# Optimization experiments

Measured on AMD Instinct MI355X. Metric: run time of the kernel, lower is better.

Reference implementation:

```python
import jax, jax.numpy as jnp
import numpy as np

_HMT = np.array([[1, 1, 1, 1], [1, -1, 1, -1], [1, 1, -1, -1], [1, -1, -1, 1]], dtype=np.float32)
_H = jnp.asarray(_HMT)
_H2 = jnp.asarray(_HMT[[1, 0, 2, 3], :])
_H3 = jnp.asarray(_HMT[[3, 1, 2, 0], :])
# inverse-transform rows 1:3 (2x4), reconstructed from truncated source
_IH = _H[1:3, :]
_IH2 = _H2[1:3, :]
_IH3 = _H3[1:3, :]

KERNEL = 4
STRIDE = 2


def setup_inputs() -> dict:
    key = jax.random.key(0)
    k1, k2, k3 = jax.random.split(key, 3)
    B, Cin, Cout, ih, iw = 16, 64, 96, 128, 128
    x = jax.random.normal(k1, (B, Cin, ih, iw), dtype=jnp.float32)
    weight = jax.random.normal(k2, (Cout, Cin, KERNEL, KERNEL), dtype=jnp.float32) * 0.05
    bias = jax.random.normal(k3, (1, Cout, 1, 1), dtype=jnp.float32) * 0.05
    return {"x": x, "weight": weight, "bias": bias}


def _extract_patches(xp, nH, nW):
    # patches[b,c,i,j,u,v] = xp[b,c, 2i+v, 2j+u]  (torch unfold(3).unfold(2) order)
    idx_h = 2 * np.arange(nH)[:, None] + np.arange(KERNEL)[None, :]  # (nH,4) over (i,v)
    idx_w = 2 * np.arange(nW)[:, None] + np.arange(KERNEL)[None, :]  # (nW,4) over (j,u)
    return xp[:, :, idx_h[:, None, None, :], idx_w[None, :, :, None]]  # (B,C,nH,nW,4,4)


def _group(t, w, ih_mat):
    # t: (B,C,nH,nW,4,4) transform-domain patches; w: (Og,C,4,4)
    m = jnp.einsum('bcijuv,ocuv->boijuv', t, w)
    # IH @ m @ IH.T -> (B,Og,nH,nW,2,2)
    return jnp.einsum('pu,boijuv,qv->boijpq', ih_mat, m, ih_mat)


def reference(x, weight, bias):
    B, Cin, ih, iw = x.shape
    Cout = weight.shape[0]
    nH, nW = ih // STRIDE, iw // STRIDE
    xp = jnp.pad(x, ((0, 0), (0, 0), (1, 1), (1, 1)))
    patches = _extract_patches(xp, nH, nW)
    # forward transforms: H @ P @ H ; H2.T @ P @ H2 ; H3.T @ P @ H3
    t1 = jnp.einsum('au,bcijuv,vd->bcijad', _H, patches, _H)
    t2 = jnp.einsum('ua,bcijuv,vd->bcijad', _H2, patches, _H2)
    t3 = jnp.einsum('ua,bcijuv,vd->bcijad', _H3, patches, _H3)
    g = Cout // 3
    h1 = _group(t1, weight[:g], _IH)
    h2 = _group(t2, weight[g:2 * g], _IH2)
    h3 = _group(t3, weight[2 * g:], _IH3)
    hmult = jnp.concatenate([h1, h2, h3], axis=1)  # (B,Cout,nH,nW,2,2)
    # out[b,o,2i+p,2j+q] = hmult[b,o,i,j,p,q]
    out = hmult.transpose(0, 1, 2, 4, 3, 5).reshape(B, Cout, ih, iw)
    return out + bias
```

## Files before the change

kernel.cpp:

```cpp
#include <hip/hip_runtime.h>
#include <hip/hip_bf16.h>
#include <cstddef>
#include <cstdint>


#define IHW 128
#define CIN 64
#define COUT 96
#define NCK 16

typedef __attribute__((ext_vector_type(8))) short short8_t;
typedef __attribute__((ext_vector_type(4))) float floatx4;

__device__ __forceinline__ short bf16r(float f) {
  uint32_t u = __float_as_uint(f);
  uint32_t r = (u + 0x7FFFu + ((u >> 16) & 1u)) >> 16;
  return (short)r;
}

__device__ __forceinline__ uint32_t pk(float lo, float hi) {
  union { __hip_bfloat16 h; unsigned short s; } a, bq;
  a.h = __float2bfloat16(lo);
  bq.h = __float2bfloat16(hi);
  return (uint32_t)a.s | ((uint32_t)bq.s << 16);
}

__global__ void keff_kernel(const float* __restrict__ w, short* __restrict__ keff) {
  int idx = blockIdx.x * 256 + threadIdx.x;
  if (idx >= COUT * CIN) return;
  int o = idx / CIN, c = idx % CIN;
  int g = o / 32;

  int perm[4] = {0, 1, 2, 3};
  if (g == 1) { perm[0] = 1; perm[1] = 0; }
  else if (g == 2) { perm[0] = 3; perm[3] = 0; }

  const float H[4][4] = {{1,1,1,1},{1,-1,1,-1},{1,1,-1,-1},{1,-1,-1,1}};
  float S[2][4];
#pragma unroll
  for (int p = 0; p < 2; ++p)
#pragma unroll
    for (int a = 0; a < 4; ++a) {
      bool pos = (g == 1) ? ((p == 0) ? true : (a < 2))
                          : ((p == 0) ? ((a & 1) == 0) : (a < 2));
      S[p][a] = pos ? 1.f : -1.f;
    }

  float wv[4][4];
#pragma unroll
  for (int a = 0; a < 4; ++a)
#pragma unroll
    for (int d = 0; d < 4; ++d) wv[a][d] = w[(o * CIN + c) * 16 + a * 4 + d];

  for (int p = 0; p < 2; ++p)
    for (int q = 0; q < 2; ++q) {
      int n = o * 4 + p * 2 + q;
      for (int y = 0; y < 4; ++y)
        for (int xx = 0; xx < 4; ++xx) {
          float s = 0.f;
#pragma unroll
          for (int a = 0; a < 4; ++a) {
            float ea = S[p][a] * H[a][perm[xx]];
#pragma unroll
            for (int d = 0; d < 4; ++d) s += ea * S[q][d] * H[d][perm[y]] * wv[a][d];
          }
          keff[n * 1024 + c * 16 + y * 4 + xx] = bf16r(s);
        }
    }
}

__global__ __launch_bounds__(256) void prepass(const float* __restrict__ x,
                                               uint32_t* __restrict__ img) {
  const int t = blockIdx.x * 256 + threadIdx.x;
  const int r = t >> 5;
  const int l = t & 31;
  const int py = r % 130;
  const int rc = r / 130;

  uint32_t d0 = 0, d1 = 0, t0 = 0;
  if (py != 0 && py != 129) {
    const float4 v = *reinterpret_cast<const float4*>(
        x + ((size_t)rc * IHW + (py - 1)) * IHW + 4 * l);
    float prev = __shfl_up(v.w, 1, 32);
    if (l == 0) prev = 0.f;
    d0 = pk(prev, v.x);
    d1 = pk(v.y, v.z);
    t0 = pk(v.w, 0.f);
  }
  uint32_t* row = img + (size_t)r * 68;
  *reinterpret_cast<uint2*>(row + 2 * l) = make_uint2(d0, d1);
  if (l == 31) *reinterpret_cast<uint4*>(row + 64) = make_uint4(t0, 0, 0, 0);
}

#define XBUF_DW 1632
#define ABUF_DW 4096

__global__ __launch_bounds__(256) void conv_mfma(const uint32_t* __restrict__ img,
                                                 const short* __restrict__ keff,
                                                 const float* __restrict__ bias,
                                                 float* __restrict__ out) {
  __shared__ uint32_t xlds[2 * XBUF_DW];
  __shared__ uint32_t alds[2 * ABUF_DW];

  const int tid = threadIdx.x;
  const int lane = tid & 63;
  const int wid = tid >> 6;
  const int wavem = wid >> 1;
  const int wn = wid & 1;
  const int l15 = lane & 15;
  const int l4 = lane >> 4;

  const int hw = blockIdx.x;
  const int xcd = hw & 7;
  const int r = hw >> 3;
  const int tile = xcd * 64 + r / 3;
  const int nblk = r % 3;
  const int b = tile >> 5;
  const int ib = tile & 31;

  const uint32_t* imgb = img + (size_t)b * CIN * 130 * 68;

  int xsrc[2];
  bool xok[2];
#pragma unroll
  for (int it = 0; it < 2; ++it) {
    const int u = wid * 102 + lane + it * 64;
    const int ri = u / 17;
    const int col16 = u % 17;
    const int kk = ri / 12;
    const int rem = ri % 12;
    const int y = rem >> 1;
    const int cs = rem & 1;
    const int cl = 2 * kk + cs;
    xsrc[it] = (cl * 130 + 4 * ib + y) * 68 + col16 * 4;
    xok[it] = (it == 0) || (lane < 38);
  }

  int aoff[4];
#pragma unroll
  for (int it = 0; it < 4; ++it) {
    const int slot = tid + it * 256;
    const int n = slot >> 3;
    const int u = slot & 7;
    aoff[it] = (nblk * 128 + n) * 1024 + ((u ^ (n & 7)) << 3);
  }

#define STAGE(bs, ckv)                                                     \
  {                                                                        \
    _Pragma("unroll") for (int it = 0; it < 4; ++it) {                     \
      const short* src = keff + aoff[it] + (ckv) * 64;                     \
      __builtin_amdgcn_global_load_lds(                                    \
          (const __attribute__((address_space(1))) void*)src,              \
          (__attribute__((address_space(3))) void*)                        \
              &alds[(bs) * ABUF_DW + (tid + it * 256) * 4],                \
          16, 0, 0);                                                       \
    }                                                                      \
    _Pragma("unroll") for (int it = 0; it < 2; ++it) {                     \
      if (xok[it]) {                                                       \
        const uint32_t* src = imgb + xsrc[it] + (ckv) * (4 * 130 * 68);    \
        __builtin_amdgcn_global_load_lds(                                  \
            (const __attribute__((address_space(1))) void*)src,            \
            (__attribute__((address_space(3))) void*)                      \
                &xlds[(bs) * XBUF_DW + (wid * 102 + it * 64) * 4],         \
            16, 0, 0);                                                     \
      }                                                                    \
    }                                                                      \
  }

  union ufrag { short8_t s8; uint32_t u[4]; };

  floatx4 acc[4][4];
#pragma unroll
  for (int i2 = 0; i2 < 4; ++i2)
#pragma unroll
    for (int j2 = 0; j2 < 4; ++j2) acc[i2][j2] = (floatx4){0.f, 0.f, 0.f, 0.f};

  float biasr[4];
#pragma unroll
  for (int nf = 0; nf < 4; ++nf) biasr[nf] = bias[nblk * 32 + wn * 16 + nf * 4 + l4];

  const int xbase = (4 * wavem + 4 * (l4 & 1) + (l4 >> 1)) * 68 + l15;
  const int abase = (wn * 64 + l15) * 32 + ((l4 ^ (l15 & 7)) << 2);

#define COMPUTE(ckv)                                                       \
  {                                                                        \
    const uint32_t* Ap = alds + ((ckv) & 1) * ABUF_DW;                     \
    const uint32_t* Xp = xlds + ((ckv) & 1) * XBUF_DW + xbase;             \
    _Pragma("unroll") for (int kk = 0; kk < 2; ++kk) {                     \
      short8_t af[4];                                                      \
      _Pragma("unroll") for (int nf = 0; nf < 4; ++nf)                     \
        af[nf] = *reinterpret_cast<const short8_t*>(                       \
            Ap + (abase ^ (kk << 4)) + nf * 512);                          \
      const uint32_t* Xk = Xp + kk * 816;                                  \
      ufrag xf[4];                                                         \
      _Pragma("unroll") for (int mf = 0; mf < 4; ++mf) {                   \
        const int o = mf * 16;                                             \
        xf[mf].u[0] = Xk[o];                                               \
        xf[mf].u[1] = Xk[o + 1];                                           \
        xf[mf].u[2] = Xk[o + 136];                                         \
        xf[mf].u[3] = Xk[o + 137];                                         \
      }                                                                    \
      _Pragma("unroll") for (int mf = 0; mf < 4; ++mf)                     \
        _Pragma("unroll") for (int nf = 0; nf < 4; ++nf)                   \
          acc[mf][nf] = __builtin_amdgcn_mfma_f32_16x16x32_bf16(           \
              af[nf], xf[mf].s8, acc[mf][nf], 0, 0, 0);                    \
    }                                                                      \
  }

  STAGE(0, 0);
  STAGE(1, 1);

  for (int ck = 0; ck < NCK - 1; ++ck) {
    asm volatile("s_waitcnt vmcnt(6) lgkmcnt(0)" ::: "memory");
    __builtin_amdgcn_s_barrier();
    __builtin_amdgcn_sched_barrier(0);
    COMPUTE(ck);
    if (ck + 2 < NCK) {
      __builtin_amdgcn_s_barrier();
      __builtin_amdgcn_sched_barrier(0);
      STAGE(ck & 1, ck + 2);
    }
  }
  asm volatile("s_waitcnt vmcnt(0) lgkmcnt(0)" ::: "memory");
  __builtin_amdgcn_s_barrier();
  __builtin_amdgcn_sched_barrier(0);
  COMPUTE(NCK - 1);

  const int i_row = ib * 2 + wavem;
  const int orow0 = 2 * i_row;
#pragma unroll
  for (int nf = 0; nf < 4; ++nf) {
    const int o = nblk * 32 + wn * 16 + nf * 4 + l4;
    const float bv = biasr[nf];
    float* obase = out + ((size_t)(b * COUT + o) * IHW + orow0) * IHW;
#pragma unroll
    for (int mf = 0; mf < 4; ++mf) {
      const int col = 2 * (mf * 16 + l15);
      float2 s0 = make_float2(acc[mf][nf][0] + bv, acc[mf][nf][1] + bv);
      float2 s1 = make_float2(acc[mf][nf][2] + bv, acc[mf][nf][3] + bv);
      *reinterpret_cast<float2*>(obase + col) = s0;
      *reinterpret_cast<float2*>(obase + IHW + col) = s1;
    }
  }
#undef STAGE
#undef COMPUTE
}

#define FB_P_DW 168
#define FB_COFF 80
#define FB_XBUF (12 * FB_P_DW)

__global__ __launch_bounds__(256) void conv_fb(const float* __restrict__ x,
                                               const short* __restrict__ keff,
                                               const float* __restrict__ bias,
                                               float* __restrict__ out) {
  __shared__ uint32_t xlds[2 * FB_XBUF];
  __shared__ uint32_t alds[2 * ABUF_DW];

  const int tid = threadIdx.x;
  const int lane = tid & 63;
  const int wid = tid >> 6;
  const int wavem = wid >> 1;
  const int wn = wid & 1;
  const int l15 = lane & 15;
  const int l4 = lane >> 4;

  const int hw = blockIdx.x;
  const int xcd = hw & 7;
  const int r = hw >> 3;
  const int tile = xcd * 64 + r / 3;
  const int nblk = r % 3;
  const int b = tile >> 5;
  const int ib = tile & 31;
  const int gy0 = ib * 4 - 1;

  const float* xb = x + (size_t)b * CIN * IHW * IHW;

  int sl_off[3], sl_dw[3], sl_s[3];
  bool sl_ok[3];
#pragma unroll
  for (int it = 0; it < 3; ++it) {
    const int slot = tid + it * 256;
    const int seg = slot >> 5;
    const int s = slot & 31;
    const int c_sub = seg / 12;
    const int rr = seg % 12;
    const int kk2 = rr / 6;
    const int y = rr % 6;
    const int c_loc = 2 * kk2 + c_sub;
    const int gy = gy0 + y;
    const bool ok = (unsigned)gy < (unsigned)IHW;
    sl_off[it] = (c_loc * IHW + (ok ? gy : 0)) * IHW + 4 * s;
    sl_dw[it] = rr * FB_P_DW + c_sub * FB_COFF;
    sl_s[it] = s;
    sl_ok[it] = ok;
  }

  int aoff[4];
#pragma unroll
  for (int it = 0; it < 4; ++it) {
    const int slot = tid + it * 256;
    const int n = slot >> 3;
    const int u = slot & 7;
    aoff[it] = (nblk * 128 + n) * 1024 + ((u ^ (n & 7)) << 3);
  }

  float4 gv[3];
  float gn[3];
#define FISSUE(ckv)                                                       \
  {                                                                       \
    _Pragma("unroll") for (int it = 0; it < 3; ++it) {                    \
      const float* p = xb + sl_off[it] + (size_t)(ckv) * (4 * IHW * IHW); \
      gv[it] = *reinterpret_cast<const float4*>(p);                       \
      gn[it] = (sl_s[it] < 31) ? p[4] : 0.f;                              \
    }                                                                     \
  }
#define FWRITE(bs)                                                        \
  {                                                                       \
    uint32_t* Bp = xlds + (bs) * FB_XBUF;                                 \
    _Pragma("unroll") for (int it = 0; it < 3; ++it) {                    \
      float4 v = gv[it];                                                  \
      float nx = gn[it];                                                  \
      if (!sl_ok[it]) { v.x = 0.f; v.y = 0.f; v.z = 0.f; v.w = 0.f; nx = 0.f; } \
      const int o = sl_dw[it] + 2 * sl_s[it] + 1;                         \
      Bp[o] = pk(v.y, v.z);                                               \
      Bp[o + 1] = pk(v.w, nx);                                            \
      if (sl_s[it] == 0) Bp[sl_dw[it]] = pk(0.f, v.x);                    \
    }                                                                     \
  }
#define FADMA(bs, ckv)                                                    \
  {                                                                       \
    _Pragma("unroll") for (int it = 0; it < 4; ++it) {                    \
      const short* src = keff + aoff[it] + (ckv) * 64;                    \
      __builtin_amdgcn_global_load_lds(                                   \
          (const __attribute__((address_space(1))) void*)src,             \
          (__attribute__((address_space(3))) void*)                       \
              &alds[(bs) * ABUF_DW + (tid + it * 256) * 4],               \
          16, 0, 0);                                                      \
    }                                                                     \
  }

  union ufragf { short8_t s8; uint32_t u[4]; };
#define FKK(Apt, Xkt, abasev)                                             \
  {                                                                       \
    short8_t af[4];                                                       \
    _Pragma("unroll") for (int nf = 0; nf < 4; ++nf)                      \
      af[nf] = *reinterpret_cast<const short8_t*>((Apt) + (abasev) + nf * 512); \
    ufragf xf[4];                                                         \
    _Pragma("unroll") for (int mf = 0; mf < 4; ++mf) {                    \
      xf[mf].u[0] = (Xkt)[mf * 16];                                       \
      xf[mf].u[1] = (Xkt)[mf * 16 + 1];                                   \
      xf[mf].u[2] = (Xkt)[mf * 16 + FB_P_DW];                             \
      xf[mf].u[3] = (Xkt)[mf * 16 + FB_P_DW + 1];                         \
    }                                                                     \
    _Pragma("unroll") for (int mf = 0; mf < 4; ++mf)                      \
      _Pragma("unroll") for (int nf = 0; nf < 4; ++nf)                    \
        acc[mf][nf] = __builtin_amdgcn_mfma_f32_16x16x32_bf16(            \
            af[nf], xf[mf].s8, acc[mf][nf], 0, 0, 0);                     \
  }

  floatx4 acc[4][4];
#pragma unroll
  for (int i2 = 0; i2 < 4; ++i2)
#pragma unroll
    for (int j2 = 0; j2 < 4; ++j2) acc[i2][j2] = (floatx4){0.f, 0.f, 0.f, 0.f};

  float biasr[4];
#pragma unroll
  for (int nf = 0; nf < 4; ++nf) biasr[nf] = bias[nblk * 32 + wn * 16 + nf * 4 + l4];

  const int cm_dw = (2 * wavem + 2 * (l4 & 1)) * FB_P_DW + (l4 >> 1) * FB_COFF + l15;
  const int a0 = (wn * 64 + l15) * 32 + ((l4 ^ (l15 & 7)) << 2);
  const int a1 = a0 ^ 16;

  FISSUE(0);
  FADMA(0, 0);
  FWRITE(0);
  FISSUE(1);

  for (int ck = 0; ck < NCK - 1; ++ck) {
    asm volatile("s_waitcnt vmcnt(6) lgkmcnt(0)" ::: "memory");
    __builtin_amdgcn_s_barrier();
    __builtin_amdgcn_sched_barrier(0);
    const int cur = ck & 1;
    const uint32_t* Ap = alds + cur * ABUF_DW;
    const uint32_t* Xk0 = xlds + cur * FB_XBUF + cm_dw;
    const uint32_t* Xk1 = Xk0 + 6 * FB_P_DW;
    FADMA(cur ^ 1, ck + 1);
    FKK(Ap, Xk0, a0);
    FKK(Ap, Xk1, a1);
    FWRITE(cur ^ 1);
    if (ck + 2 < NCK) FISSUE(ck + 2);
  }
  asm volatile("s_waitcnt vmcnt(0) lgkmcnt(0)" ::: "memory");
  __builtin_amdgcn_s_barrier();
  __builtin_amdgcn_sched_barrier(0);
  {
    const uint32_t* Ap = alds + ABUF_DW;
    const uint32_t* Xk0 = xlds + FB_XBUF + cm_dw;
    const uint32_t* Xk1 = Xk0 + 6 * FB_P_DW;
    FKK(Ap, Xk0, a0);
    FKK(Ap, Xk1, a1);
  }

  const int i_row = ib * 2 + wavem;
  const int orow0 = 2 * i_row;
#pragma unroll
  for (int nf = 0; nf < 4; ++nf) {
    const int o = nblk * 32 + wn * 16 + nf * 4 + l4;
    const float bv = biasr[nf];
    float* obase = out + ((size_t)(b * COUT + o) * IHW + orow0) * IHW;
#pragma unroll
    for (int mf = 0; mf < 4; ++mf) {
      const int col = 2 * (mf * 16 + l15);
      float2 s0 = make_float2(acc[mf][nf][0] + bv, acc[mf][nf][1] + bv);
      float2 s1 = make_float2(acc[mf][nf][2] + bv, acc[mf][nf][3] + bv);
      *reinterpret_cast<float2*>(obase + col) = s0;
      *reinterpret_cast<float2*>(obase + IHW + col) = s1;
    }
  }
#undef FISSUE
#undef FWRITE
#undef FADMA
#undef FKK
}

extern "C" void kernel_launch(void* const* d_in, const int* in_sizes, int n_in,
                              void* d_out, int out_size, void* d_ws, size_t ws_size,
                              hipStream_t stream) {
  const float* x = (const float*)d_in[0];
  const float* w = (const float*)d_in[1];
  const float* bias = (const float*)d_in[2];
  float* out = (float*)d_out;
  short* keff = (short*)d_ws;
  uint32_t* img = (uint32_t*)((char*)d_ws + 786432);

  const size_t NEED = 786432 + (size_t)16 * 64 * 130 * 272;

  hipLaunchKernelGGL(keff_kernel, dim3(24), dim3(256), 0, stream, w, keff);
  if (ws_size >= NEED) {
    hipLaunchKernelGGL(prepass, dim3(16640), dim3(256), 0, stream, x, img);
    hipLaunchKernelGGL(conv_mfma, dim3(1536), dim3(256), 0, stream, img, keff, bias, out);
  } else {
    hipLaunchKernelGGL(conv_fb, dim3(1536), dim3(256), 0, stream, x, keff, bias, out);
  }
}
```

Measured before the change: 84.55 us.

## Fuse weight and image prep kernels; triple-buffer weights with one barrier per step

The weight-transform and image-prepass kernels are merged into a single launch, with blocks dispatched by index, to remove one kernel launch and its gap. In the main MFMA conv kernel, the weight tile buffer grows from double to triple buffering and the image tile is staged one step ahead, so each K-step needs only one barrier instead of two. The next loads are issued before the compute of the current step to overlap global-to-LDS copies with MFMA work. The larger LDS footprint (about 61KB) may reduce how many blocks fit on each CU.

```diff
diff --git a/kernel.cpp b/kernel.cpp
--- a/kernel.cpp
+++ b/kernel.cpp
@@ -25,53 +25,58 @@
   return (uint32_t)a.s | ((uint32_t)bq.s << 16);
 }
 
-__global__ void keff_kernel(const float* __restrict__ w, short* __restrict__ keff) {
-  int idx = blockIdx.x * 256 + threadIdx.x;
-  if (idx >= COUT * CIN) return;
-  int o = idx / CIN, c = idx % CIN;
-  int g = o / 32;
-
-  int perm[4] = {0, 1, 2, 3};
-  if (g == 1) { perm[0] = 1; perm[1] = 0; }
-  else if (g == 2) { perm[0] = 3; perm[3] = 0; }
-
-  const float H[4][4] = {{1,1,1,1},{1,-1,1,-1},{1,1,-1,-1},{1,-1,-1,1}};
-  float S[2][4];
-#pragma unroll
-  for (int p = 0; p < 2; ++p)
-#pragma unroll
-    for (int a = 0; a < 4; ++a) {
-      bool pos = (g == 1) ? ((p == 0) ? true : (a < 2))
-                          : ((p == 0) ? ((a & 1) == 0) : (a < 2));
-      S[p][a] = pos ? 1.f : -1.f;
-    }
-
-  float wv[4][4];
-#pragma unroll
-  for (int a = 0; a < 4; ++a)
-#pragma unroll
-    for (int d = 0; d < 4; ++d) wv[a][d] = w[(o * CIN + c) * 16 + a * 4 + d];
-
-  for (int p = 0; p < 2; ++p)
-    for (int q = 0; q < 2; ++q) {
-      int n = o * 4 + p * 2 + q;
-      for (int y = 0; y < 4; ++y)
-        for (int xx = 0; xx < 4; ++xx) {
-          float s = 0.f;
-#pragma unroll
-          for (int a = 0; a < 4; ++a) {
-            float ea = S[p][a] * H[a][perm[xx]];
-#pragma unroll
-            for (int d = 0; d < 4; ++d) s += ea * S[q][d] * H[d][perm[y]] * wv[a][d];
+__global__ __launch_bounds__(256) void prep_all(const float* __restrict__ x,
+                                                const float* __restrict__ w,
+                                                uint32_t* __restrict__ img,
+                                                short* __restrict__ keff,
+                                                int do_img) {
+  if (blockIdx.x < 24) {
+    int idx = blockIdx.x * 256 + threadIdx.x;
+    if (idx >= COUT * CIN) return;
+    int o = idx / CIN, c = idx % CIN;
+    int g = o / 32;
+
+    int perm[4] = {0, 1, 2, 3};
+    if (g == 1) { perm[0] = 1; perm[1] = 0; }
+    else if (g == 2) { perm[0] = 3; perm[3] = 0; }
+
+    const float H[4][4] = {{1,1,1,1},{1,-1,1,-1},{1,1,-1,-1},{1,-1,-1,1}};
+    float S[2][4];
+#pragma unroll
+    for (int p = 0; p < 2; ++p)
+#pragma unroll
+      for (int a = 0; a < 4; ++a) {
+        bool pos = (g == 1) ? ((p == 0) ? true : (a < 2))
+                            : ((p == 0) ? ((a & 1) == 0) : (a < 2));
+        S[p][a] = pos ? 1.f : -1.f;
+      }
+
+    float wv[4][4];
+#pragma unroll
+    for (int a = 0; a < 4; ++a)
+#pragma unroll
+      for (int d = 0; d < 4; ++d) wv[a][d] = w[(o * CIN + c) * 16 + a * 4 + d];
+
+    for (int p = 0; p < 2; ++p)
+      for (int q = 0; q < 2; ++q) {
+        int n = o * 4 + p * 2 + q;
+        for (int y = 0; y < 4; ++y)
+          for (int xx = 0; xx < 4; ++xx) {
+            float s = 0.f;
+#pragma unroll
+            for (int a = 0; a < 4; ++a) {
+              float ea = S[p][a] * H[a][perm[xx]];
+#pragma unroll
+              for (int d = 0; d < 4; ++d) s += ea * S[q][d] * H[d][perm[y]] * wv[a][d];
+            }
+            keff[n * 1024 + c * 16 + y * 4 + xx] = bf16r(s);
           }
-          keff[n * 1024 + c * 16 + y * 4 + xx] = bf16r(s);
-        }
-    }
-}
-
-__global__ __launch_bounds__(256) void prepass(const float* __restrict__ x,
-                                               uint32_t* __restrict__ img) {
-  const int t = blockIdx.x * 256 + threadIdx.x;
+      }
+    return;
+  }
+  if (!do_img) return;
+
+  const int t = (blockIdx.x - 24) * 256 + threadIdx.x;
   const int r = t >> 5;
   const int l = t & 31;
   const int py = r % 130;
@@ -100,7 +105,7 @@
                                                  const float* __restrict__ bias,
                                                  float* __restrict__ out) {
   __shared__ uint32_t xlds[2 * XBUF_DW];
-  __shared__ uint32_t alds[2 * ABUF_DW];
+  __shared__ uint32_t alds[3 * ABUF_DW];
 
   const int tid = threadIdx.x;
   const int lane = tid & 63;
@@ -145,7 +150,7 @@
     aoff[it] = (nblk * 128 + n) * 1024 + ((u ^ (n & 7)) << 3);
   }
 
-#define STAGE(bs, ckv)                                                     \
+#define STAGE_A(bs, ckv)                                                   \
   {                                                                        \
     _Pragma("unroll") for (int it = 0; it < 4; ++it) {                     \
       const short* src = keff + aoff[it] + (ckv) * 64;                     \
@@ -155,6 +160,10 @@
               &alds[(bs) * ABUF_DW + (tid + it * 256) * 4],                \
           16, 0, 0);                                                       \
     }                                                                      \
+  }
+
+#define STAGE_X(bs, ckv)                                                   \
+  {                                                                        \
     _Pragma("unroll") for (int it = 0; it < 2; ++it) {                     \
       if (xok[it]) {                                                       \
         const uint32_t* src = imgb + xsrc[it] + (ckv) * (4 * 130 * 68);    \
@@ -182,10 +191,10 @@
   const int xbase = (4 * wavem + 4 * (l4 & 1) + (l4 >> 1)) * 68 + l15;
   const int abase = (wn * 64 + l15) * 32 + ((l4 ^ (l15 & 7)) << 2);
 
-#define COMPUTE(ckv)                                                       \
+#define COMPUTE(Apt, Xpt)                                                  \
   {                                                                        \
-    const uint32_t* Ap = alds + ((ckv) & 1) * ABUF_DW;                     \
-    const uint32_t* Xp = xlds + ((ckv) & 1) * XBUF_DW + xbase;             \
+    const uint32_t* Ap = (Apt);                                            \
+    const uint32_t* Xp = (Xpt) + xbase;                                    \
     _Pragma("unroll") for (int kk = 0; kk < 2; ++kk) {                     \
       short8_t af[4];                                                      \
       _Pragma("unroll") for (int nf = 0; nf < 4; ++nf)                     \
@@ -207,24 +216,34 @@
     }                                                                      \
   }
 
-  STAGE(0, 0);
-  STAGE(1, 1);
-
+  STAGE_X(0, 0);
+  __builtin_amdgcn_sched_barrier(0);
+  STAGE_A(0, 0);
+  STAGE_A(1, 1);
+  __builtin_amdgcn_sched_barrier(0);
+
+  int acur = 0;
   for (int ck = 0; ck < NCK - 1; ++ck) {
-    asm volatile("s_waitcnt vmcnt(6) lgkmcnt(0)" ::: "memory");
+    asm volatile("s_waitcnt vmcnt(4)" ::: "memory");
     __builtin_amdgcn_s_barrier();
     __builtin_amdgcn_sched_barrier(0);
-    COMPUTE(ck);
+
+    STAGE_X((ck + 1) & 1, ck + 1);
+    __builtin_amdgcn_sched_barrier(0);
     if (ck + 2 < NCK) {
-      __builtin_amdgcn_s_barrier();
+      const int astg = (acur >= 1) ? acur - 1 : acur + 2;
+      STAGE_A(astg, ck + 2);
       __builtin_amdgcn_sched_barrier(0);
-      STAGE(ck & 1, ck + 2);
     }
-  }
-  asm volatile("s_waitcnt vmcnt(0) lgkmcnt(0)" ::: "memory");
+
+    COMPUTE(alds + acur * ABUF_DW, xlds + (ck & 1) * XBUF_DW);
+    acur = (acur == 2) ? 0 : acur + 1;
+  }
+
+  asm volatile("s_waitcnt vmcnt(0)" ::: "memory");
   __builtin_amdgcn_s_barrier();
   __builtin_amdgcn_sched_barrier(0);
-  COMPUTE(NCK - 1);
+  COMPUTE(alds + acur * ABUF_DW, xlds + ((NCK - 1) & 1) * XBUF_DW);
 
   const int i_row = ib * 2 + wavem;
   const int orow0 = 2 * i_row;
@@ -242,7 +261,8 @@
       *reinterpret_cast<float2*>(obase + IHW + col) = s1;
     }
   }
-#undef STAGE
+#undef STAGE_A
+#undef STAGE_X
 #undef COMPUTE
 }
 
@@ -436,10 +456,11 @@
   uint32_t* img = (uint32_t*)((char*)d_ws + 786432);
 
   const size_t NEED = 786432 + (size_t)16 * 64 * 130 * 272;
-
-  hipLaunchKernelGGL(keff_kernel, dim3(24), dim3(256), 0, stream, w, keff);
-  if (ws_size >= NEED) {
-    hipLaunchKernelGGL(prepass, dim3(16640), dim3(256), 0, stream, x, img);
+  const bool big = ws_size >= NEED;
+
+  hipLaunchKernelGGL(prep_all, dim3(big ? 16664 : 24), dim3(256), 0, stream,
+                     x, w, img, keff, big ? 1 : 0);
+  if (big) {
     hipLaunchKernelGGL(conv_mfma, dim3(1536), dim3(256), 0, stream, img, keff, bias, out);
   } else {
     hipLaunchKernelGGL(conv_fb, dim3(1536), dim3(256), 0, stream, x, keff, bias, out);
```

New measurement: 87.91 us. +4.0%, slower.

## Merge prep kernels and deepen conv pipeline to 4 stages with smaller K chunks

Applied to the files above, without the earlier changes.

Fuses the keff and image prepass kernels into a single launch, removing one kernel launch and its gap. The conv_mfma main loop moves from 16 chunks of two MFMA k-steps with two buffers to 32 half-size chunks with a four-buffer ring. Each iteration issues loads for two chunks ahead before waiting, and one barrier per iteration replaces two. In exchange there are more barriers overall, smaller loads per chunk, and a changed LDS swizzle that could add bank conflicts.

```diff
diff --git a/kernel.cpp b/kernel.cpp
--- a/kernel.cpp
+++ b/kernel.cpp
@@ -7,7 +7,9 @@
 #define IHW 128
 #define CIN 64
 #define COUT 96
-#define NCK 16
+#define NCK 32
+#define XB_DW 816
+#define AB_DW 2048
 
 typedef __attribute__((ext_vector_type(8))) short short8_t;
 typedef __attribute__((ext_vector_type(4))) float floatx4;
@@ -25,53 +27,58 @@
   return (uint32_t)a.s | ((uint32_t)bq.s << 16);
 }
 
-__global__ void keff_kernel(const float* __restrict__ w, short* __restrict__ keff) {
-  int idx = blockIdx.x * 256 + threadIdx.x;
-  if (idx >= COUT * CIN) return;
-  int o = idx / CIN, c = idx % CIN;
-  int g = o / 32;
-
-  int perm[4] = {0, 1, 2, 3};
-  if (g == 1) { perm[0] = 1; perm[1] = 0; }
-  else if (g == 2) { perm[0] = 3; perm[3] = 0; }
-
-  const float H[4][4] = {{1,1,1,1},{1,-1,1,-1},{1,1,-1,-1},{1,-1,-1,1}};
-  float S[2][4];
-#pragma unroll
-  for (int p = 0; p < 2; ++p)
-#pragma unroll
-    for (int a = 0; a < 4; ++a) {
-      bool pos = (g == 1) ? ((p == 0) ? true : (a < 2))
-                          : ((p == 0) ? ((a & 1) == 0) : (a < 2));
-      S[p][a] = pos ? 1.f : -1.f;
-    }
-
-  float wv[4][4];
-#pragma unroll
-  for (int a = 0; a < 4; ++a)
-#pragma unroll
-    for (int d = 0; d < 4; ++d) wv[a][d] = w[(o * CIN + c) * 16 + a * 4 + d];
-
-  for (int p = 0; p < 2; ++p)
-    for (int q = 0; q < 2; ++q) {
-      int n = o * 4 + p * 2 + q;
-      for (int y = 0; y < 4; ++y)
-        for (int xx = 0; xx < 4; ++xx) {
-          float s = 0.f;
-#pragma unroll
-          for (int a = 0; a < 4; ++a) {
-            float ea = S[p][a] * H[a][perm[xx]];
-#pragma unroll
-            for (int d = 0; d < 4; ++d) s += ea * S[q][d] * H[d][perm[y]] * wv[a][d];
+__global__ __launch_bounds__(256) void prep_all(const float* __restrict__ x,
+                                                const float* __restrict__ w,
+                                                uint32_t* __restrict__ img,
+                                                short* __restrict__ keff,
+                                                int do_img) {
+  if (blockIdx.x < 24) {
+    int idx = blockIdx.x * 256 + threadIdx.x;
+    if (idx >= COUT * CIN) return;
+    int o = idx / CIN, c = idx % CIN;
+    int g = o / 32;
+
+    int perm[4] = {0, 1, 2, 3};
+    if (g == 1) { perm[0] = 1; perm[1] = 0; }
+    else if (g == 2) { perm[0] = 3; perm[3] = 0; }
+
+    const float H[4][4] = {{1,1,1,1},{1,-1,1,-1},{1,1,-1,-1},{1,-1,-1,1}};
+    float S[2][4];
+#pragma unroll
+    for (int p = 0; p < 2; ++p)
+#pragma unroll
+      for (int a = 0; a < 4; ++a) {
+        bool pos = (g == 1) ? ((p == 0) ? true : (a < 2))
+                            : ((p == 0) ? ((a & 1) == 0) : (a < 2));
+        S[p][a] = pos ? 1.f : -1.f;
+      }
+
+    float wv[4][4];
+#pragma unroll
+    for (int a = 0; a < 4; ++a)
+#pragma unroll
+      for (int d = 0; d < 4; ++d) wv[a][d] = w[(o * CIN + c) * 16 + a * 4 + d];
+
+    for (int p = 0; p < 2; ++p)
+      for (int q = 0; q < 2; ++q) {
+        int n = o * 4 + p * 2 + q;
+        for (int y = 0; y < 4; ++y)
+          for (int xx = 0; xx < 4; ++xx) {
+            float s = 0.f;
+#pragma unroll
+            for (int a = 0; a < 4; ++a) {
+              float ea = S[p][a] * H[a][perm[xx]];
+#pragma unroll
+              for (int d = 0; d < 4; ++d) s += ea * S[q][d] * H[d][perm[y]] * wv[a][d];
+            }
+            keff[n * 1024 + c * 16 + y * 4 + xx] = bf16r(s);
           }
-          keff[n * 1024 + c * 16 + y * 4 + xx] = bf16r(s);
-        }
-    }
-}
-
-__global__ __launch_bounds__(256) void prepass(const float* __restrict__ x,
-                                               uint32_t* __restrict__ img) {
-  const int t = blockIdx.x * 256 + threadIdx.x;
+      }
+    return;
+  }
+  if (!do_img) return;
+
+  const int t = (blockIdx.x - 24) * 256 + threadIdx.x;
   const int r = t >> 5;
   const int l = t & 31;
   const int py = r % 130;
@@ -92,15 +99,12 @@
   if (l == 31) *reinterpret_cast<uint4*>(row + 64) = make_uint4(t0, 0, 0, 0);
 }
 
-#define XBUF_DW 1632
-#define ABUF_DW 4096
-
 __global__ __launch_bounds__(256) void conv_mfma(const uint32_t* __restrict__ img,
                                                  const short* __restrict__ keff,
                                                  const float* __restrict__ bias,
                                                  float* __restrict__ out) {
-  __shared__ uint32_t xlds[2 * XBUF_DW];
-  __shared__ uint32_t alds[2 * ABUF_DW];
+  __shared__ uint32_t alds[4 * AB_DW];
+  __shared__ uint32_t xlds[4 * XB_DW];
 
   const int tid = threadIdx.x;
   const int lane = tid & 63;
@@ -120,50 +124,42 @@
 
   const uint32_t* imgb = img + (size_t)b * CIN * 130 * 68;
 
-  int xsrc[2];
-  bool xok[2];
+  int xsrc = 0;
+  const bool xact = tid < 204;
+  {
+    const int ri = tid / 17;
+    const int col16 = tid % 17;
+    const int y = ri >> 1;
+    const int cs = ri & 1;
+    xsrc = (cs * 130 + 4 * ib + y) * 68 + col16 * 4;
+  }
+
+  int asrc[2];
 #pragma unroll
   for (int it = 0; it < 2; ++it) {
-    const int u = wid * 102 + lane + it * 64;
-    const int ri = u / 17;
-    const int col16 = u % 17;
-    const int kk = ri / 12;
-    const int rem = ri % 12;
-    const int y = rem >> 1;
-    const int cs = rem & 1;
-    const int cl = 2 * kk + cs;
-    xsrc[it] = (cl * 130 + 4 * ib + y) * 68 + col16 * 4;
-    xok[it] = (it == 0) || (lane < 38);
-  }
-
-  int aoff[4];
-#pragma unroll
-  for (int it = 0; it < 4; ++it) {
     const int slot = tid + it * 256;
-    const int n = slot >> 3;
-    const int u = slot & 7;
-    aoff[it] = (nblk * 128 + n) * 1024 + ((u ^ (n & 7)) << 3);
+    const int n = slot >> 2;
+    const int p = slot & 3;
+    asrc[it] = (nblk * 128 + n) * 1024 + ((p ^ ((n >> 1) & 3)) << 3);
   }
 
 #define STAGE(bs, ckv)                                                     \
   {                                                                        \
-    _Pragma("unroll") for (int it = 0; it < 4; ++it) {                     \
-      const short* src = keff + aoff[it] + (ckv) * 64;                     \
+    _Pragma("unroll") for (int it = 0; it < 2; ++it) {                     \
+      const short* src = keff + asrc[it] + (ckv) * 32;                     \
       __builtin_amdgcn_global_load_lds(                                    \
           (const __attribute__((address_space(1))) void*)src,              \
           (__attribute__((address_space(3))) void*)                        \
-              &alds[(bs) * ABUF_DW + (tid + it * 256) * 4],                \
+              &alds[(bs) * AB_DW + (tid + it * 256) * 4],                  \
           16, 0, 0);                                                       \
     }                                                                      \
-    _Pragma("unroll") for (int it = 0; it < 2; ++it) {                     \
-      if (xok[it]) {                                                       \
-        const uint32_t* src = imgb + xsrc[it] + (ckv) * (4 * 130 * 68);    \
-        __builtin_amdgcn_global_load_lds(                                  \
-            (const __attribute__((address_space(1))) void*)src,            \
-            (__attribute__((address_space(3))) void*)                      \
-                &xlds[(bs) * XBUF_DW + (wid * 102 + it * 64) * 4],         \
-            16, 0, 0);                                                     \
-      }                                                                    \
+    if (xact) {                                                            \
+      const uint32_t* src = imgb + xsrc + (ckv) * (2 * 130 * 68);          \
+      __builtin_amdgcn_global_load_lds(                                    \
+          (const __attribute__((address_space(1))) void*)src,              \
+          (__attribute__((address_space(3))) void*)                        \
+              &xlds[(bs) * XB_DW + tid * 4],                               \
+          16, 0, 0);                                                       \
     }                                                                      \
   }
 
@@ -179,49 +175,47 @@
 #pragma unroll
   for (int nf = 0; nf < 4; ++nf) biasr[nf] = bias[nblk * 32 + wn * 16 + nf * 4 + l4];
 
+  const int abase = (wn * 64 + l15) * 16 + ((l4 ^ ((l15 >> 1) & 3)) << 2);
   const int xbase = (4 * wavem + 4 * (l4 & 1) + (l4 >> 1)) * 68 + l15;
-  const int abase = (wn * 64 + l15) * 32 + ((l4 ^ (l15 & 7)) << 2);
 
 #define COMPUTE(ckv)                                                       \
   {                                                                        \
-    const uint32_t* Ap = alds + ((ckv) & 1) * ABUF_DW;                     \
-    const uint32_t* Xp = xlds + ((ckv) & 1) * XBUF_DW + xbase;             \
-    _Pragma("unroll") for (int kk = 0; kk < 2; ++kk) {                     \
-      short8_t af[4];                                                      \
+    const uint32_t* Ap = alds + ((ckv) & 3) * AB_DW;                       \
+    const uint32_t* Xp = xlds + ((ckv) & 3) * XB_DW + xbase;               \
+    short8_t af[4];                                                        \
+    _Pragma("unroll") for (int nf = 0; nf < 4; ++nf)                       \
+      af[nf] = *reinterpret_cast<const short8_t*>(Ap + abase + nf * 256);  \
+    ufrag xf[4];                                                           \
+    _Pragma("unroll") for (int mf = 0; mf < 4; ++mf) {                     \
+      const int o = mf * 16;                                               \
+      xf[mf].u[0] = Xp[o];                                                 \
+      xf[mf].u[1] = Xp[o + 1];                                             \
+      xf[mf].u[2] = Xp[o + 136];                                           \
+      xf[mf].u[3] = Xp[o + 137];                                           \
+    }                                                                      \
+    _Pragma("unroll") for (int mf = 0; mf < 4; ++mf)                       \
       _Pragma("unroll") for (int nf = 0; nf < 4; ++nf)                     \
-        af[nf] = *reinterpret_cast<const short8_t*>(                       \
-            Ap + (abase ^ (kk << 4)) + nf * 512);                          \
-      const uint32_t* Xk = Xp + kk * 816;                                  \
-      ufrag xf[4];                                                         \
-      _Pragma("unroll") for (int mf = 0; mf < 4; ++mf) {                   \
-        const int o = mf * 16;                                             \
-        xf[mf].u[0] = Xk[o];                                               \
-        xf[mf].u[1] = Xk[o + 1];                                           \
-        xf[mf].u[2] = Xk[o + 136];                                         \
-        xf[mf].u[3] = Xk[o + 137];                                         \
-      }                                                                    \
-      _Pragma("unroll") for (int mf = 0; mf < 4; ++mf)                     \
-        _Pragma("unroll") for (int nf = 0; nf < 4; ++nf)                   \
-          acc[mf][nf] = __builtin_amdgcn_mfma_f32_16x16x32_bf16(           \
-              af[nf], xf[mf].s8, acc[mf][nf], 0, 0, 0);                    \
-    }                                                                      \
+        acc[mf][nf] = __builtin_amdgcn_mfma_f32_16x16x32_bf16(             \
+            af[nf], xf[mf].s8, acc[mf][nf], 0, 0, 0);                      \
   }
 
   STAGE(0, 0);
+  __builtin_amdgcn_sched_barrier(0);
   STAGE(1, 1);
-
-  for (int ck = 0; ck < NCK - 1; ++ck) {
-    asm volatile("s_waitcnt vmcnt(6) lgkmcnt(0)" ::: "memory");
+  __builtin_amdgcn_sched_barrier(0);
+
+  for (int ck = 0; ck < NCK - 2; ++ck) {
+    STAGE((ck + 2) & 3, ck + 2);
+    asm volatile("s_waitcnt vmcnt(6)" ::: "memory");
     __builtin_amdgcn_s_barrier();
     __builtin_amdgcn_sched_barrier(0);
     COMPUTE(ck);
-    if (ck + 2 < NCK) {
-      __builtin_amdgcn_s_barrier();
-      __builtin_amdgcn_sched_barrier(0);
-      STAGE(ck & 1, ck + 2);
-    }
-  }
-  asm volatile("s_waitcnt vmcnt(0) lgkmcnt(0)" ::: "memory");
+  }
+  asm volatile("s_waitcnt vmcnt(3)" ::: "memory");
+  __builtin_amdgcn_s_barrier();
+  __builtin_amdgcn_sched_barrier(0);
+  COMPUTE(NCK - 2);
+  asm volatile("s_waitcnt vmcnt(0)" ::: "memory");
   __builtin_amdgcn_s_barrier();
   __builtin_amdgcn_sched_barrier(0);
   COMPUTE(NCK - 1);
@@ -249,13 +243,14 @@
 #define FB_P_DW 168
 #define FB_COFF 80
 #define FB_XBUF (12 * FB_P_DW)
+#define FB_ABUF 4096
 
 __global__ __launch_bounds__(256) void conv_fb(const float* __restrict__ x,
                                                const short* __restrict__ keff,
                                                const float* __restrict__ bias,
                                                float* __restrict__ out) {
   __shared__ uint32_t xlds[2 * FB_XBUF];
-  __shared__ uint32_t alds[2 * ABUF_DW];
+  __shared__ uint32_t alds[2 * FB_ABUF];
 
   const int tid = threadIdx.x;
   const int lane = tid & 63;
@@ -335,7 +330,7 @@
       __builtin_amdgcn_global_load_lds(                                   \
           (const __attribute__((address_space(1))) void*)src,             \
           (__attribute__((address_space(3))) void*)                       \
-              &alds[(bs) * ABUF_DW + (tid + it * 256) * 4],               \
+              &alds[(bs) * FB_ABUF + (tid + it * 256) * 4],               \
           16, 0, 0);                                                      \
     }                                                                     \
   }
@@ -378,25 +373,25 @@
   FWRITE(0);
   FISSUE(1);
 
-  for (int ck = 0; ck < NCK - 1; ++ck) {
+  for (int ck = 0; ck < 16 - 1; ++ck) {
     asm volatile("s_waitcnt vmcnt(6) lgkmcnt(0)" ::: "memory");
     __builtin_amdgcn_s_barrier();
     __builtin_amdgcn_sched_barrier(0);
     const int cur = ck & 1;
-    const uint32_t* Ap = alds + cur * ABUF_DW;
+    const uint32_t* Ap = alds + cur * FB_ABUF;
     const uint32_t* Xk0 = xlds + cur * FB_XBUF + cm_dw;
     const uint32_t* Xk1 = Xk0 + 6 * FB_P_DW;
     FADMA(cur ^ 1, ck + 1);
     FKK(Ap, Xk0, a0);
     FKK(Ap, Xk1, a1);
     FWRITE(cur ^ 1);
-    if (ck + 2 < NCK) FISSUE(ck + 2);
+    if (ck + 2 < 16) FISSUE(ck + 2);
   }
   asm volatile("s_waitcnt vmcnt(0) lgkmcnt(0)" ::: "memory");
   __builtin_amdgcn_s_barrier();
   __builtin_amdgcn_sched_barrier(0);
   {
-    const uint32_t* Ap = alds + ABUF_DW;
+    const uint32_t* Ap = alds + FB_ABUF;
     const uint32_t* Xk0 = xlds + FB_XBUF + cm_dw;
     const uint32_t* Xk1 = Xk0 + 6 * FB_P_DW;
     FKK(Ap, Xk0, a0);
@@ -436,10 +431,11 @@
   uint32_t* img = (uint32_t*)((char*)d_ws + 786432);
 
   const size_t NEED = 786432 + (size_t)16 * 64 * 130 * 272;
-
-  hipLaunchKernelGGL(keff_kernel, dim3(24), dim3(256), 0, stream, w, keff);
-  if (ws_size >= NEED) {
-    hipLaunchKernelGGL(prepass, dim3(16640), dim3(256), 0, stream, x, img);
+  const bool big = ws_size >= NEED;
+
+  hipLaunchKernelGGL(prep_all, dim3(big ? 16664 : 24), dim3(256), 0, stream,
+                     x, w, img, keff, big ? 1 : 0);
+  if (big) {
     hipLaunchKernelGGL(conv_mfma, dim3(1536), dim3(256), 0, stream, img, keff, bias, out);
   } else {
     hipLaunchKernelGGL(conv_fb, dim3(1536), dim3(256), 0, stream, x, keff, bias, out);
```

Measured after the change: 86.15 us. No clear change (+1.9%).
